# Performance work log

Measured on AMD Instinct MI355X. Metric: run time of the kernel, lower is better.

The kernel has to match this reference:

```python
import jax, jax.numpy as jnp
import numpy as np

RHO = 1060.0   # blood density kg/m^3
DX = 1e-3      # grid spacing
CCFL = 0.9     # CFL number
EPS_A = 1e-6   # area floor


def setup_inputs() -> dict:
    key = jax.random.key(0)
    k0, k1, k2 = jax.random.split(key, 3)
    M = 90000          # 3 vessels x 30000 cells
    T = 150            # time steps
    Rs = jax.random.normal(k0, (4,), dtype=jnp.float32)
    sim_dat = jnp.ones((2, M), dtype=jnp.float32)            # row0: A, row1: Q seed
    sim_dat_const = jax.random.uniform(k1, (11, M), dtype=jnp.float32)
    input_data = jax.random.uniform(k2, (T,), dtype=jnp.float32)
    strides = jnp.array([[0, 30000], [30000, 60000], [60000, 90000]], dtype=jnp.int32)
    return {"Rs": Rs, "sim_dat": sim_dat, "sim_dat_const": sim_dat_const,
            "input_data": input_data, "strides": strides, "upper": T}


def reference(Rs, sim_dat, sim_dat_const, input_data, strides, upper):
    M = sim_dat.shape[1]
    # --- SimDense: softplus reparam of 4 resistance scale factors ---
    rs = jax.nn.softplus(Rs)
    idx = jnp.arange(M)
    m1 = (idx >= strides[1, 0]) & (idx < strides[1, 1])  # vessel 1 region
    m2 = (idx >= strides[2, 0]) & (idx < strides[2, 1])  # vessel 2 region
    # constant rows (shifted positive)
    A0 = sim_dat_const[0] + 0.5     # reference area
    beta = sim_dat_const[1] + 1.0   # wall stiffness
    R1 = sim_dat_const[7] + 0.5     # proximal resistance (VAR_INDEX_1)
    R2 = sim_dat_const[8] + 0.5     # distal resistance (VAR_INDEX_2)
    # scatter scaled resistances into vessel-1 / vessel-2 regions
    R1 = jnp.where(m1, rs[0] * R1, jnp.where(m2, rs[2] * R1, R1))
    R2 = jnp.where(m1, rs[1] * R2, jnp.where(m2, rs[3] * R2, R2))
    Rtot = R1 + R2

    A_init = sim_dat[0]
    Q_init = 0.1 * sim_dat[1]
    starts = strides[:, 0]
    ends = strides[:, 1] - 1
    mids = (strides[:, 0] + strides[:, 1]) // 2

    def step(carry, inflow):
        A, Q = carry
        A = jnp.maximum(A, EPS_A)
        sq = jnp.sqrt(A / A0)
        P = beta * (sq - 1.0)                 # tube-law pressure
        u = Q / A
        c = jnp.sqrt(0.5 * beta / RHO * sq)   # wave speed
        smax = jnp.max(jnp.abs(u) + c)
        dt = CCFL * DX / smax                 # CFL-limited timestep
        # conservative fluxes for (A, Q)
        F_A = Q
        F_Q = Q * u + beta / (3.0 * RHO * A0) * A * sq
        # Lax-Friedrichs interface fluxes
        fhA = 0.5 * (F_A[:-1] + F_A[1:]) - 0.5 * smax * (A[1:] - A[:-1])
        fhQ = 0.5 * (F_Q[:-1] + F_Q[1:]) - 0.5 * smax * (Q[1:] - Q[:-1])
        lam = dt / DX
        A_new = A.at[1:-1].add(-lam * (fhA[1:] - fhA[:-1]))
        Q_new = Q.at[1:-1].add(-lam * (fhQ[1:] - fhQ[:-1]))
        # inlet / junction BC: prescribed inflow at each vessel start
        Q_new = Q_new.at[starts].set(inflow)
        # outlet BC: resistive Windkessel Q = P / (R1 + R2)
        Q_new = Q_new.at[ends].set(P[ends] / Rtot[ends])
        A_new = jnp.maximum(A_new, EPS_A)
        return (A_new, Q_new), P[mids]          # record mid-vessel pressures

    _, p = jax.lax.scan(step, (A_init, Q_init), input_data)
    return p  # [upper, 3]
```

## Files before the change

kernel.cpp:

```cpp
#include <hip/hip_runtime.h>

static constexpr int MM  = 90000;
static constexpr int TT  = 150;
static constexpr int BS  = 256;
static constexpr int CPT = 4;
static constexpr int CPB = BS * CPT;
static constexpr int NB  = (MM + CPB - 1) / CPB;
static constexpr int WPB = BS / 64;
static constexpr int NWAVE  = NB * WPB;
static constexpr int WPAGES = 384;
static constexpr int PAGE_U32 = 2048;
static constexpr int PAGE_U64 = 1024;

__device__ unsigned int       g_wmax[WPAGES][PAGE_U32];
__device__ unsigned long long g_edge_s[NB][PAGE_U64];
__device__ unsigned long long g_dummy64;

__device__ __forceinline__ float softplus_f(float x) {
    return fmaxf(x, 0.0f) + log1pf(expf(-fabsf(x)));
}
__device__ __forceinline__ unsigned long long packAQ(float A, float Q) {
    return ((unsigned long long)__float_as_uint(Q) << 32) | (unsigned long long)__float_as_uint(A);
}
#define AG_LOAD32(p)     __hip_atomic_load((p), __ATOMIC_RELAXED, __HIP_MEMORY_SCOPE_AGENT)
#define AG_LOAD64(p)     __hip_atomic_load((p), __ATOMIC_RELAXED, __HIP_MEMORY_SCOPE_AGENT)
#define AG_STORE32(p, v) __hip_atomic_store((p), (v), __ATOMIC_RELAXED, __HIP_MEMORY_SCOPE_AGENT)
#define AG_STORE64(p, v) __hip_atomic_store((p), (v), __ATOMIC_RELAXED, __HIP_MEMORY_SCOPE_AGENT)

#define DPP_MAX(x, ctrl, rm, bm)                                                     \
    x = fmaxf(x, __int_as_float(__builtin_amdgcn_update_dpp(                          \
                     0, __float_as_int(x), (ctrl), (rm), (bm), true)))
__device__ __forceinline__ float wave_max64(float x) {
    DPP_MAX(x, 0x111, 0xf, 0xf);
    DPP_MAX(x, 0x112, 0xf, 0xf);
    DPP_MAX(x, 0x114, 0xf, 0xe);
    DPP_MAX(x, 0x118, 0xf, 0xc);
    DPP_MAX(x, 0x142, 0xa, 0xf);
    DPP_MAX(x, 0x143, 0xc, 0xf);
    return x;
}

__global__ void init_ws_kernel() {
    int i = blockIdx.x * blockDim.x + threadIdx.x;
    int stride = gridDim.x * blockDim.x;
    unsigned int* pw = &g_wmax[0][0];
    for (int j = i; j < WPAGES * PAGE_U32; j += stride)
        pw[j] = ((j / PAGE_U32) < NWAVE) ? 0u : 1u;
    unsigned long long* pe = &g_edge_s[0][0];
    for (int j = i; j < NB * PAGE_U64; j += stride) pe[j] = 0ull;
    if (i == 0) g_dummy64 = ~0ull;
}

__global__ void __launch_bounds__(BS) sim_kernel(
    const float* __restrict__ Rs,
    const float* __restrict__ sim_dat,
    const float* __restrict__ sdc,
    const float* __restrict__ inflow,
    float* __restrict__ out)
{
    __shared__ float sE[2][WPB][2][3];
    __shared__ float s_bc[2];
    __shared__ float s_hL[3], s_hR[3];
    __shared__ float s_inflow[TT];

    const int b    = blockIdx.x;
    const int tid  = threadIdx.x;
    const int wv   = tid >> 6;
    const int lane = tid & 63;
    const int base = b * CPB + tid * CPT;
    const int gw   = b * WPB + wv;

    for (int j = tid; j < TT; j += BS) s_inflow[j] = inflow[j];

    float A[CPT], Q[CPT], A0v[CPT], bet[CPT], cbv[CPT], k2v[CPT], sq[CPT], FQ[CPT];
    bool  act[CPT];
    #pragma unroll
    for (int c = 0; c < CPT; ++c) {
        int i = base + c;
        act[c] = (i < MM);
        if (act[c]) {
            A[c]   = fmaxf(sim_dat[i], 1e-6f);
            Q[c]   = 0.1f * sim_dat[MM + i];
            A0v[c] = sdc[i] + 0.5f;
            bet[c] = sdc[MM + i] + 1.0f;
        } else { A[c] = 1.0f; Q[c] = 0.0f; A0v[c] = 1.0f; bet[c] = 1.0f; }
        cbv[c] = (0.5f * bet[c]) / 1060.0f;
        k2v[c] = bet[c] / (3180.0f * A0v[c]);
    }
    const bool isStart = (base == 0) | (base == 30000) | (base == 60000);
    const bool isEnd   = (base + 3 == 29999) | (base + 3 == 59999) | (base + 3 == 89999);
    const int midSlot = (base == 15000) ? 0 : (base == 45000) ? 1 : (base == 75000) ? 2 : -1;
    float Rtot = 1.0f;
    if (isEnd) {
        int i3 = base + 3;
        float R1 = sdc[7 * MM + i3] + 0.5f;
        float R2 = sdc[8 * MM + i3] + 0.5f;
        if (i3 == 59999)      { R1 *= softplus_f(Rs[0]); R2 *= softplus_f(Rs[1]); }
        else if (i3 == 89999) { R1 *= softplus_f(Rs[2]); R2 *= softplus_f(Rs[3]); }
        Rtot = R1 + R2;
    }

    const bool pubL = (tid == 0) && (b > 0);
    const bool pubR = (tid == BS - 1) && (b < NB - 1);

    const unsigned int* pwl = &g_wmax[lane][0];

    float s4 = 0.0f;
    #pragma unroll
    for (int c = 0; c < CPT; ++c) {
        sq[c] = sqrtf(A[c] / A0v[c]);
        float uu = Q[c] / A[c];
        float cc = sqrtf(cbv[c] * sq[c]);
        FQ[c] = Q[c] * uu + k2v[c] * A[c] * sq[c];
        s4 = fmaxf(s4, act[c] ? (fabsf(uu) + cc) : 0.0f);
    }
    if (pubL) {
        AG_STORE64(&g_edge_s[b][0], packAQ(A[0], Q[0]));
        AG_STORE64(&g_edge_s[b][1], (unsigned long long)__float_as_uint(FQ[0]));
    }
    if (pubR) {
        AG_STORE64(&g_edge_s[b][2], packAQ(A[3], Q[3]));
        AG_STORE64(&g_edge_s[b][3], (unsigned long long)__float_as_uint(FQ[3]));
    }
    {
        float red = wave_max64(s4);
        if (lane == 63) AG_STORE32(&g_wmax[gw][0], __float_as_uint(red));
    }
    if (lane == 0)       { sE[0][wv][0][0] = A[0]; sE[0][wv][0][1] = Q[0]; sE[0][wv][0][2] = FQ[0]; }
    else if (lane == 63) { sE[0][wv][1][0] = A[3]; sE[0][wv][1][1] = Q[3]; sE[0][wv][1][2] = FQ[3]; }

    for (int t = 0; t < TT; ++t) {
        const int par = t & 1, npar = par ^ 1;

        unsigned int x0, x1, x2, x3, x4, x5;
        unsigned long long e64;
        const unsigned long long* pE = &g_dummy64;
        if (wv == 0) {
            const int t4 = t * 4;
            if (lane == 0 && b > 0)           pE = &g_edge_s[b - 1][t4 + 2];
            else if (lane == 1 && b > 0)      pE = &g_edge_s[b - 1][t4 + 3];
            else if (lane == 2 && b < NB - 1) pE = &g_edge_s[b + 1][t4 + 0];
            else if (lane == 3 && b < NB - 1) pE = &g_edge_s[b + 1][t4 + 1];
            const unsigned int* p = pwl + t;
            x0 = AG_LOAD32(p);
            x1 = AG_LOAD32(p +  64 * PAGE_U32);
            x2 = AG_LOAD32(p + 128 * PAGE_U32);
            x3 = AG_LOAD32(p + 192 * PAGE_U32);
            x4 = AG_LOAD32(p + 256 * PAGE_U32);
            x5 = AG_LOAD32(p + 320 * PAGE_U32);
            e64 = AG_LOAD64(pE);
        }

        float Am = __shfl_up(A[3], 1, 64),  Qm = __shfl_up(Q[3], 1, 64),  Fm = __shfl_up(FQ[3], 1, 64);
        float Ap = __shfl_down(A[0], 1, 64), Qp = __shfl_down(Q[0], 1, 64), Fp = __shfl_down(FQ[0], 1, 64);

        float dFA[CPT], lapA[CPT], dFQ[CPT], lapQ[CPT];
        #pragma unroll
        for (int c = 0; c < CPT; ++c) {
            float Al = (c == 0) ? Am : A[c-1],  Ql = (c == 0) ? Qm : Q[c-1],  Fl = (c == 0) ? Fm : FQ[c-1];
            float Ar = (c == 3) ? Ap : A[c+1],  Qr = (c == 3) ? Qp : Q[c+1],  Fr = (c == 3) ? Fp : FQ[c+1];
            dFA[c]  = 0.5f * (Qr - Ql);
            lapA[c] = 0.5f * (Ar - 2.0f * A[c] + Al);
            dFQ[c]  = 0.5f * (Fr - Fl);
            lapQ[c] = 0.5f * (Qr - 2.0f * Q[c] + Ql);
        }
        if (midSlot >= 0) out[t * 3 + midSlot] = bet[0] * (sq[0] - 1.0f);
        float qFix = 0.0f;
        if (isStart) qFix = s_inflow[t];
        if (isEnd)   qFix = (bet[3] * (sq[3] - 1.0f)) / Rtot;

        if (wv == 0) {
            const unsigned int* p = pwl + t;
            bool ok = __all((x0 != 0u) & (x1 != 0u) & (x2 != 0u) & (x3 != 0u) &
                            (x4 != 0u) & (x5 != 0u) & (e64 != 0ull));
            while (!ok) {
                x0 = AG_LOAD32(p);
                x1 = AG_LOAD32(p +  64 * PAGE_U32);
                x2 = AG_LOAD32(p + 128 * PAGE_U32);
                x3 = AG_LOAD32(p + 192 * PAGE_U32);
                x4 = AG_LOAD32(p + 256 * PAGE_U32);
                x5 = AG_LOAD32(p + 320 * PAGE_U32);
                e64 = AG_LOAD64(pE);
                ok = __all((x0 != 0u) & (x1 != 0u) & (x2 != 0u) & (x3 != 0u) &
                           (x4 != 0u) & (x5 != 0u) & (e64 != 0ull));
            }
            if (lane == 0 && b > 0)           { s_hL[0] = __uint_as_float((unsigned int)e64);
                                                s_hL[1] = __uint_as_float((unsigned int)(e64 >> 32)); }
            else if (lane == 1 && b > 0)      { s_hL[2] = __uint_as_float((unsigned int)e64); }
            else if (lane == 2 && b < NB - 1) { s_hR[0] = __uint_as_float((unsigned int)e64);
                                                s_hR[1] = __uint_as_float((unsigned int)(e64 >> 32)); }
            else if (lane == 3 && b < NB - 1) { s_hR[2] = __uint_as_float((unsigned int)e64); }
            float m = fmaxf(fmaxf(fmaxf(__uint_as_float(x0), __uint_as_float(x1)),
                                  fmaxf(__uint_as_float(x2), __uint_as_float(x3))),
                            fmaxf(__uint_as_float(x4), __uint_as_float(x5)));
            m = wave_max64(m);
            const float smax = __int_as_float(__builtin_amdgcn_readlane(__float_as_int(m), 63));
            const float dt  = ((float)(0.9 * 0.001)) / smax;
            const float lam = dt / 0.001f;
            const float w   = lam * smax;
            if (lane == 0) { s_bc[0] = lam; s_bc[1] = w; }
        }
        __syncthreads();
        const float lam = s_bc[0];
        const float w   = s_bc[1];

        if (lane == 0 && (wv > 0 || b > 0)) {
            float Al, Ql, Fl;
            if (wv > 0) { Al = sE[par][wv-1][1][0]; Ql = sE[par][wv-1][1][1]; Fl = sE[par][wv-1][1][2]; }
            else        { Al = s_hL[0];             Ql = s_hL[1];             Fl = s_hL[2]; }
            dFA[0]  = 0.5f * (Q[1] - Ql);
            lapA[0] = 0.5f * (A[1] - 2.0f * A[0] + Al);
            dFQ[0]  = 0.5f * (FQ[1] - Fl);
            lapQ[0] = 0.5f * (Q[1] - 2.0f * Q[0] + Ql);
        }
        if (lane == 63 && (wv < WPB - 1 || b < NB - 1)) {
            float Ar, Qr, Fr;
            if (wv < WPB - 1) { Ar = sE[par][wv+1][0][0]; Qr = sE[par][wv+1][0][1]; Fr = sE[par][wv+1][0][2]; }
            else              { Ar = s_hR[0];             Qr = s_hR[1];             Fr = s_hR[2]; }
            dFA[3]  = 0.5f * (Qr - Q[2]);
            lapA[3] = 0.5f * (Ar - 2.0f * A[3] + A[2]);
            dFQ[3]  = 0.5f * (Fr - FQ[2]);
            lapQ[3] = 0.5f * (Qr - 2.0f * Q[3] + Q[2]);
        }

        #pragma unroll
        for (int c = 0; c < CPT; ++c) {
            int i = base + c;
            if (act[c] && i > 0 && i < MM - 1) {
                A[c] = fmaf(w, lapA[c], fmaf(-lam, dFA[c], A[c]));
                Q[c] = fmaf(w, lapQ[c], fmaf(-lam, dFQ[c], Q[c]));
            }
        }
        if (isStart) Q[0] = qFix;
        if (isEnd)   Q[3] = qFix;
        #pragma unroll
        for (int c = 0; c < CPT; ++c) A[c] = fmaxf(A[c], 1e-6f);

        const int n4 = (t + 1) * 4;
        if (pubL) AG_STORE64(&g_edge_s[b][n4 + 0], packAQ(A[0], Q[0]));
        if (pubR) AG_STORE64(&g_edge_s[b][n4 + 2], packAQ(A[3], Q[3]));

        float uu[CPT];
        s4 = 0.0f;
        #pragma unroll
        for (int c = 0; c < CPT; ++c) {
            sq[c] = sqrtf(A[c] / A0v[c]);
            uu[c] = Q[c] / A[c];
            float cc = sqrtf(cbv[c] * sq[c]);
            s4 = fmaxf(s4, act[c] ? (fabsf(uu[c]) + cc) : 0.0f);
        }
        {
            float red = wave_max64(s4);
            if (lane == 63) AG_STORE32(&g_wmax[gw][t + 1], __float_as_uint(red));
        }
        #pragma unroll
        for (int c = 0; c < CPT; ++c)
            FQ[c] = Q[c] * uu[c] + k2v[c] * A[c] * sq[c];

        if (pubL) AG_STORE64(&g_edge_s[b][n4 + 1], (unsigned long long)__float_as_uint(FQ[0]));
        if (pubR) AG_STORE64(&g_edge_s[b][n4 + 3], (unsigned long long)__float_as_uint(FQ[3]));

        if (lane == 0)       { sE[npar][wv][0][0] = A[0]; sE[npar][wv][0][1] = Q[0]; sE[npar][wv][0][2] = FQ[0]; }
        else if (lane == 63) { sE[npar][wv][1][0] = A[3]; sE[npar][wv][1][1] = Q[3]; sE[npar][wv][1][2] = FQ[3]; }
    }
}

extern "C" void kernel_launch(void* const* d_in, const int* in_sizes, int n_in,
                              void* d_out, int out_size, void* d_ws, size_t ws_size,
                              hipStream_t stream) {
    (void)in_sizes; (void)n_in; (void)d_ws; (void)ws_size; (void)out_size;

    const float* Rs      = (const float*)d_in[0];
    const float* sim_dat = (const float*)d_in[1];
    const float* sdc     = (const float*)d_in[2];
    const float* inflow  = (const float*)d_in[3];
    float* out = (float*)d_out;

    hipLaunchKernelGGL(init_ws_kernel, dim3(240), dim3(256), 0, stream);

    hipLaunchKernelGGL(sim_kernel, dim3(NB), dim3(BS), 0, stream,
                       Rs, sim_dat, sdc, inflow, out);
}
```

Measured before the change: 459.9 us.

## Pipeline spin-wait polling with inline-asm double-buffered loads and guard

Replaces the atomic-load spin loop, which waited on the cross-block wave-max and edge flags, with inline-asm global loads using the sc1 cache bit. Two sets of seven loads are kept in flight alternately, so each poll check overlaps the next round trip. It also replaces __syncthreads with a raw barrier after an LDS waitcnt, and moves the dt/lam computation to every thread. A guard counter with a shared panic flag lets blocks exit instead of hanging, at the risk of silently wrong results if the guard trips.

Result: no change. 464.1 us (+0.9%).

```diff
diff --git a/kernel.cpp b/kernel.cpp
--- a/kernel.cpp
+++ b/kernel.cpp
@@ -7,13 +7,16 @@
 static constexpr int CPB = BS * CPT;
 static constexpr int NB  = (MM + CPB - 1) / CPB;
 static constexpr int WPB = BS / 64;
-static constexpr int NWAVE  = NB * WPB;
+static constexpr int NWAVE = NB * WPB;
 static constexpr int WPAGES = 384;
 static constexpr int PAGE_U32 = 2048;
 static constexpr int PAGE_U64 = 1024;
-
-__device__ unsigned int       g_wmax[WPAGES][PAGE_U32];
-__device__ unsigned long long g_edge_s[NB][PAGE_U64];
+static constexpr int GUARD_MAX = 4096;
+
+typedef unsigned int u32x2 __attribute__((ext_vector_type(2)));
+
+__device__ __attribute__((aligned(128))) unsigned int       g_wmax[WPAGES][PAGE_U32];
+__device__ __attribute__((aligned(128))) unsigned long long g_edge_s[NB][PAGE_U64];
 __device__ unsigned long long g_dummy64;
 
 __device__ __forceinline__ float softplus_f(float x) {
@@ -22,13 +25,35 @@
 __device__ __forceinline__ unsigned long long packAQ(float A, float Q) {
     return ((unsigned long long)__float_as_uint(Q) << 32) | (unsigned long long)__float_as_uint(A);
 }
-#define AG_LOAD32(p)     __hip_atomic_load((p), __ATOMIC_RELAXED, __HIP_MEMORY_SCOPE_AGENT)
-#define AG_LOAD64(p)     __hip_atomic_load((p), __ATOMIC_RELAXED, __HIP_MEMORY_SCOPE_AGENT)
 #define AG_STORE32(p, v) __hip_atomic_store((p), (v), __ATOMIC_RELAXED, __HIP_MEMORY_SCOPE_AGENT)
 #define AG_STORE64(p, v) __hip_atomic_store((p), (v), __ATOMIC_RELAXED, __HIP_MEMORY_SCOPE_AGENT)
 
-#define DPP_MAX(x, ctrl, rm, bm)                                                     \
-    x = fmaxf(x, __int_as_float(__builtin_amdgcn_update_dpp(                          \
+#define ISSUE7(x0,x1,x2,x3,x4,x5,e,p0,p1,p2,p3,p4,p5,pe)                        \
+    asm volatile("global_load_dword %0, %7, off sc1\n\t"                        \
+                 "global_load_dword %1, %8, off sc1\n\t"                        \
+                 "global_load_dword %2, %9, off sc1\n\t"                        \
+                 "global_load_dword %3, %10, off sc1\n\t"                       \
+                 "global_load_dword %4, %11, off sc1\n\t"                       \
+                 "global_load_dword %5, %12, off sc1\n\t"                       \
+                 "global_load_dwordx2 %6, %13, off sc1"                         \
+                 : "=&v"(x0),"=&v"(x1),"=&v"(x2),"=&v"(x3),"=&v"(x4),"=&v"(x5),"=&v"(e) \
+                 : "v"(p0),"v"(p1),"v"(p2),"v"(p3),"v"(p4),"v"(p5),"v"(pe)      \
+                 : "memory")
+#define WAIT7_TIE(x0,x1,x2,x3,x4,x5,e)                                          \
+    do { asm volatile("s_waitcnt vmcnt(7)"                                      \
+             : "+v"(x0),"+v"(x1),"+v"(x2),"+v"(x3),"+v"(x4),"+v"(x5),"+v"(e)    \
+             :: "memory");                                                      \
+         __builtin_amdgcn_sched_barrier(0); } while (0)
+#define CHK7(x0,x1,x2,x3,x4,x5,e)                                               \
+    __all(((x0) != 0u) & ((x1) != 0u) & ((x2) != 0u) & ((x3) != 0u) &           \
+          ((x4) != 0u) & ((x5) != 0u) & ((e).x != 0u))
+#define FENCE_LDS() asm volatile("s_waitcnt lgkmcnt(0)" ::: "memory")
+#define BAR() do { FENCE_LDS();                                                 \
+                   __builtin_amdgcn_s_barrier();                                \
+                   __builtin_amdgcn_sched_barrier(0); } while (0)
+
+#define DPP_MAX(x, ctrl, rm, bm)                                                \
+    x = fmaxf(x, __int_as_float(__builtin_amdgcn_update_dpp(                    \
                      0, __float_as_int(x), (ctrl), (rm), (bm), true)))
 __device__ __forceinline__ float wave_max64(float x) {
     DPP_MAX(x, 0x111, 0xf, 0xf);
@@ -45,7 +70,7 @@
     int stride = gridDim.x * blockDim.x;
     unsigned int* pw = &g_wmax[0][0];
     for (int j = i; j < WPAGES * PAGE_U32; j += stride)
-        pw[j] = ((j / PAGE_U32) < NWAVE) ? 0u : 1u;
+        pw[j] = ((j >> 11) < NWAVE) ? 0u : 1u;
     unsigned long long* pe = &g_edge_s[0][0];
     for (int j = i; j < NB * PAGE_U64; j += stride) pe[j] = 0ull;
     if (i == 0) g_dummy64 = ~0ull;
@@ -59,9 +84,10 @@
     float* __restrict__ out)
 {
     __shared__ float sE[2][WPB][2][3];
-    __shared__ float s_bc[2];
+    __shared__ float s_smaxv;
     __shared__ float s_hL[3], s_hR[3];
     __shared__ float s_inflow[TT];
+    __shared__ int   s_panic;
 
     const int b    = blockIdx.x;
     const int tid  = threadIdx.x;
@@ -71,6 +97,7 @@
     const int gw   = b * WPB + wv;
 
     for (int j = tid; j < TT; j += BS) s_inflow[j] = inflow[j];
+    if (tid == 0) s_panic = 0;
 
     float A[CPT], Q[CPT], A0v[CPT], bet[CPT], cbv[CPT], k2v[CPT], sq[CPT], FQ[CPT];
     bool  act[CPT];
@@ -103,8 +130,6 @@
     const bool pubL = (tid == 0) && (b > 0);
     const bool pubR = (tid == BS - 1) && (b < NB - 1);
 
-    const unsigned int* pwl = &g_wmax[lane][0];
-
     float s4 = 0.0f;
     #pragma unroll
     for (int c = 0; c < CPT; ++c) {
@@ -132,23 +157,21 @@
     for (int t = 0; t < TT; ++t) {
         const int par = t & 1, npar = par ^ 1;
 
-        unsigned int x0, x1, x2, x3, x4, x5;
-        unsigned long long e64;
-        const unsigned long long* pE = &g_dummy64;
+        unsigned int b0, b1, b2, b3, b4, b5, c0, c1, c2, c3, c4, c5;
+        u32x2 bE, cE;
+        const unsigned int *p0, *p1, *p2, *p3, *p4, *p5;
+        const unsigned long long* pE;
         if (wv == 0) {
+            p0 = &g_wmax[lane      ][t];  p1 = &g_wmax[lane +  64][t];
+            p2 = &g_wmax[lane + 128][t];  p3 = &g_wmax[lane + 192][t];
+            p4 = &g_wmax[lane + 256][t];  p5 = &g_wmax[lane + 320][t];
             const int t4 = t * 4;
+            pE = &g_dummy64;
             if (lane == 0 && b > 0)           pE = &g_edge_s[b - 1][t4 + 2];
             else if (lane == 1 && b > 0)      pE = &g_edge_s[b - 1][t4 + 3];
             else if (lane == 2 && b < NB - 1) pE = &g_edge_s[b + 1][t4 + 0];
             else if (lane == 3 && b < NB - 1) pE = &g_edge_s[b + 1][t4 + 1];
-            const unsigned int* p = pwl + t;
-            x0 = AG_LOAD32(p);
-            x1 = AG_LOAD32(p +  64 * PAGE_U32);
-            x2 = AG_LOAD32(p + 128 * PAGE_U32);
-            x3 = AG_LOAD32(p + 192 * PAGE_U32);
-            x4 = AG_LOAD32(p + 256 * PAGE_U32);
-            x5 = AG_LOAD32(p + 320 * PAGE_U32);
-            e64 = AG_LOAD64(pE);
+            ISSUE7(b0, b1, b2, b3, b4, b5, bE, p0, p1, p2, p3, p4, p5, pE);
         }
 
         float Am = __shfl_up(A[3], 1, 64),  Qm = __shfl_up(Q[3], 1, 64),  Fm = __shfl_up(FQ[3], 1, 64);
@@ -170,39 +193,40 @@
         if (isEnd)   qFix = (bet[3] * (sq[3] - 1.0f)) / Rtot;
 
         if (wv == 0) {
-            const unsigned int* p = pwl + t;
-            bool ok = __all((x0 != 0u) & (x1 != 0u) & (x2 != 0u) & (x3 != 0u) &
-                            (x4 != 0u) & (x5 != 0u) & (e64 != 0ull));
-            while (!ok) {
-                x0 = AG_LOAD32(p);
-                x1 = AG_LOAD32(p +  64 * PAGE_U32);
-                x2 = AG_LOAD32(p + 128 * PAGE_U32);
-                x3 = AG_LOAD32(p + 192 * PAGE_U32);
-                x4 = AG_LOAD32(p + 256 * PAGE_U32);
-                x5 = AG_LOAD32(p + 320 * PAGE_U32);
-                e64 = AG_LOAD64(pE);
-                ok = __all((x0 != 0u) & (x1 != 0u) & (x2 != 0u) & (x3 != 0u) &
-                           (x4 != 0u) & (x5 != 0u) & (e64 != 0ull));
+            ISSUE7(c0, c1, c2, c3, c4, c5, cE, p0, p1, p2, p3, p4, p5, pE);
+            WAIT7_TIE(b0, b1, b2, b3, b4, b5, bE);
+            if (!CHK7(b0, b1, b2, b3, b4, b5, bE)) {
+                int guard = 0;
+                for (;;) {
+                    ISSUE7(b0, b1, b2, b3, b4, b5, bE, p0, p1, p2, p3, p4, p5, pE);
+                    WAIT7_TIE(c0, c1, c2, c3, c4, c5, cE);
+                    if (CHK7(c0, c1, c2, c3, c4, c5, cE)) {
+                        b0=c0; b1=c1; b2=c2; b3=c3; b4=c4; b5=c5; bE=cE; break;
+                    }
+                    ISSUE7(c0, c1, c2, c3, c4, c5, cE, p0, p1, p2, p3, p4, p5, pE);
+                    WAIT7_TIE(b0, b1, b2, b3, b4, b5, bE);
+                    if (CHK7(b0, b1, b2, b3, b4, b5, bE)) break;
+                    if (++guard >= GUARD_MAX) { if (lane == 0) s_panic = 1; break; }
+                }
             }
-            if (lane == 0 && b > 0)           { s_hL[0] = __uint_as_float((unsigned int)e64);
-                                                s_hL[1] = __uint_as_float((unsigned int)(e64 >> 32)); }
-            else if (lane == 1 && b > 0)      { s_hL[2] = __uint_as_float((unsigned int)e64); }
-            else if (lane == 2 && b < NB - 1) { s_hR[0] = __uint_as_float((unsigned int)e64);
-                                                s_hR[1] = __uint_as_float((unsigned int)(e64 >> 32)); }
-            else if (lane == 3 && b < NB - 1) { s_hR[2] = __uint_as_float((unsigned int)e64); }
-            float m = fmaxf(fmaxf(fmaxf(__uint_as_float(x0), __uint_as_float(x1)),
-                                  fmaxf(__uint_as_float(x2), __uint_as_float(x3))),
-                            fmaxf(__uint_as_float(x4), __uint_as_float(x5)));
+            if (lane == 0 && b > 0)           { s_hL[0] = __uint_as_float(bE.x);
+                                                s_hL[1] = __uint_as_float(bE.y); }
+            else if (lane == 1 && b > 0)      { s_hL[2] = __uint_as_float(bE.x); }
+            else if (lane == 2 && b < NB - 1) { s_hR[0] = __uint_as_float(bE.x);
+                                                s_hR[1] = __uint_as_float(bE.y); }
+            else if (lane == 3 && b < NB - 1) { s_hR[2] = __uint_as_float(bE.x); }
+            float m = fmaxf(fmaxf(fmaxf(__uint_as_float(b0), __uint_as_float(b1)),
+                                  fmaxf(__uint_as_float(b2), __uint_as_float(b3))),
+                            fmaxf(__uint_as_float(b4), __uint_as_float(b5)));
             m = wave_max64(m);
-            const float smax = __int_as_float(__builtin_amdgcn_readlane(__float_as_int(m), 63));
-            const float dt  = ((float)(0.9 * 0.001)) / smax;
-            const float lam = dt / 0.001f;
-            const float w   = lam * smax;
-            if (lane == 0) { s_bc[0] = lam; s_bc[1] = w; }
-        }
-        __syncthreads();
-        const float lam = s_bc[0];
-        const float w   = s_bc[1];
+            if (lane == 63) s_smaxv = __int_as_float(__builtin_amdgcn_readlane(__float_as_int(m), 63));
+        }
+        BAR();
+        if (s_panic) break;
+        const float smax = s_smaxv;
+        const float dt  = ((float)(0.9 * 0.001)) / smax;
+        const float lam = dt / 0.001f;
+        const float w   = lam * smax;
 
         if (lane == 0 && (wv > 0 || b > 0)) {
             float Al, Ql, Fl;
```
